# Optimization experiments

Measured on AMD Instinct MI355X. Metric: run time of the kernel, lower is better.

## Reference

```python
import jax, jax.numpy as jnp
import numpy as np

B = 32
T, F1, F2 = 128, 8, 8          # input_shape
N_PATCHES = 1024               # (128/4)*(8/1)*(8/2)
INPUT_D = 8                    # 4*1*2
D = 64                         # hidden_d
H = 8                          # n_heads
DH = D // H                    # d_head = 8
S = N_PATCHES + 1              # sequence length with class token
OUT_D = 9
EPS = 1e-5


def _pos_emb(seq_len, d):
    # Faithful to the original (including the odd-index formula precedence):
    # even j: sin(i / 10000**(j/d));  odd j: cos(i / (10000**(j-1) / d))
    i = np.arange(seq_len, dtype=np.float64)[:, None]
    j = np.arange(d, dtype=np.float64)[None, :]
    even = np.sin(i / np.power(10000.0, j / d))
    odd = np.cos(i / (np.power(10000.0, j - 1.0) / d))
    return jnp.asarray(np.where(j.astype(np.int64) % 2 == 0, even, odd), dtype=jnp.float32)


def _layernorm2d(x, gamma, beta):
    # nn.LayerNorm((S, D)): normalize over the last TWO dims, affine [S, D]
    mu = jnp.mean(x, axis=(-2, -1), keepdims=True)
    var = jnp.mean((x - mu) ** 2, axis=(-2, -1), keepdims=True)
    return (x - mu) * jax.lax.rsqrt(var + EPS) * gamma + beta


def setup_inputs() -> dict:
    key = jax.random.key(0)
    ks = jax.random.split(key, 18)
    sc = 0.05
    return {
        "images": jax.random.normal(ks[0], (B, T, F1, F2), jnp.float32),
        "w_map": jax.random.normal(ks[1], (INPUT_D, D), jnp.float32) * sc,
        "b_map": jax.random.normal(ks[2], (D,), jnp.float32) * sc,
        "cls_tok": jax.random.uniform(ks[3], (1, D), jnp.float32),
        "g1": jnp.ones((S, D), jnp.float32),
        "be1": jnp.zeros((S, D), jnp.float32),
        "wq": jax.random.normal(ks[4], (H, DH, DH), jnp.float32) * sc,
        "bq": jax.random.normal(ks[5], (H, DH), jnp.float32) * sc,
        "wk": jax.random.normal(ks[6], (H, DH, DH), jnp.float32) * sc,
        "bk": jax.random.normal(ks[7], (H, DH), jnp.float32) * sc,
        "wv": jax.random.normal(ks[8], (H, DH, DH), jnp.float32) * sc,
        "bv": jax.random.normal(ks[9], (H, DH), jnp.float32) * sc,
        "g2": jnp.ones((S, D), jnp.float32),
        "be2": jnp.zeros((S, D), jnp.float32),
        "w_enc": jax.random.normal(ks[10], (D, D), jnp.float32) * sc,
        "b_enc": jax.random.normal(ks[11], (D,), jnp.float32) * sc,
        "w_out": jax.random.normal(ks[12], (D, OUT_D), jnp.float32) * sc,
        "b_out": jax.random.normal(ks[13], (OUT_D,), jnp.float32) * sc,
    }


def _msa(x, wq, bq, wk, bk, wv, bv):
    # x: [B, S, D] -> per-head linear QKV, softmax attention, concat heads
    b, s, _ = x.shape
    xh = x.reshape(b, s, H, DH)                                   # [B,S,H,dh]
    q = jnp.einsum("bshd,hde->bshe", xh, wq) + bq
    k = jnp.einsum("bshd,hde->bshe", xh, wk) + bk
    v = jnp.einsum("bshd,hde->bshe", xh, wv) + bv
    scores = jnp.einsum("bqhe,bkhe->bhqk", q, k) / (DH ** 0.5)    # [B,H,S,S]
    attn = jax.nn.softmax(scores, axis=-1)
    out = jnp.einsum("bhqk,bkhe->bqhe", attn, v)                  # [B,S,H,dh]
    return out.reshape(b, s, D)


def reference(images, w_map, b_map, cls_tok, g1, be1, wq, bq, wk, bk, wv, bv,
              g2, be2, w_enc, b_enc, w_out, b_out):
    n = images.shape[0]
    patches = images.reshape(n, N_PATCHES, INPUT_D)
    tokens = patches @ w_map + b_map                              # [B,P,D]
    cls = jnp.broadcast_to(cls_tok[None, :, :], (n, 1, D))
    tokens = jnp.concatenate([cls, tokens], axis=1)               # [B,S,D]
    tokens = tokens + _pos_emb(S, D)[None, :, :]
    out = tokens + _msa(_layernorm2d(tokens, g1, be1), wq, bq, wk, bk, wv, bv)
    out = out + jax.nn.relu(_layernorm2d(out, g2, be2) @ w_enc + b_enc)
    h = out[:, 0]                                                 # class token
    return jax.nn.softmax(h @ w_out + b_out, axis=-1)
```

## Files before the change

### kernel.cpp

```cpp
#include <hip/hip_runtime.h>
#include <math.h>

#define BB 32
#define SS 1025
#define DD 64
#define HH 8
#define IN_D 8
#define NPATCH 1024
#define OUTD 9
#define EPSF 1e-5f
#define SD (SS*DD)
#define SP 1056
#define NQT 65
#define NCH 33
#define VTROW 1064
#define NTB 257
#define ZROW 1055

typedef __attribute__((ext_vector_type(8))) short bf16x8;
typedef __attribute__((ext_vector_type(4))) float f32x4;
typedef __attribute__((ext_vector_type(4))) unsigned u32x4;

#define SCALE_LOG2E (0.35355339059327378f * 1.4426950408889634f)

#if __has_builtin(__builtin_amdgcn_exp2f)
__device__ __forceinline__ float exp2_fast(float x) { return __builtin_amdgcn_exp2f(x); }
#else
__device__ __forceinline__ float exp2_fast(float x) {
    float r; asm("v_exp_f32 %0, %1" : "=v"(r) : "v"(x)); return r;
}
#endif

__device__ __forceinline__ short f2bf(float f) {
    union { float f; unsigned u; } a; a.f = f;
    unsigned r = a.u + 0x7FFFu + ((a.u >> 16) & 1u);
    return (short)(r >> 16);
}

__device__ __forceinline__ unsigned cvt_pk_bf16(float lo, float hi) {
    unsigned r;
    asm("v_cvt_pk_bf16_f32 %0, %1, %2" : "=v"(r) : "v"(lo), "v"(hi));
    return r;
}

__device__ __forceinline__ int sigmaPV(int v) {
    return ((v & 24) >> 1) | (v & 3) | ((v & 4) << 2);
}

__global__ void k_tokens(const float* __restrict__ images, const float* __restrict__ w_map,
                         const float* __restrict__ b_map, const float* __restrict__ cls,
                         float* __restrict__ tokens, float* __restrict__ part1,
                         float* __restrict__ partq1, float* __restrict__ sum2,
                         float* __restrict__ sumsq2) {
    int b = blockIdx.y;
    int bx = blockIdx.x;
    int idx = bx * 256 + threadIdx.x;
    int tid = threadIdx.x;
    __shared__ float recip[64];
    __shared__ float sh[512];
    if (tid < 64) {
        int j = tid;
        float div;
        if ((j & 1) == 0)
            div = powf(10000.0f, (float)j * (1.0f / 64.0f));
        else
            div = powf(10000.0f, (float)(j - 1)) * (1.0f / 64.0f);
        recip[j] = 1.0f / div;
    }
    __syncthreads();
    float lv = 0.f, lvv = 0.f;
    if (idx < SD) {
        int s = idx >> 6, j = idx & 63;
        float arg = (float)s * recip[j];
        float pv = (j & 1) ? __cosf(arg) : __sinf(arg);
        float v;
        if (s == 0) {
            v = cls[j];
        } else {
            const float* p = images + (size_t)b * (NPATCH * IN_D) + (size_t)(s - 1) * IN_D;
            float acc = b_map[j];
#pragma unroll
            for (int i = 0; i < IN_D; ++i) acc += p[i] * w_map[i * DD + j];
            v = acc;
        }
        v += pv;
        tokens[(size_t)b * SD + idx] = v;
        lv = v; lvv = v * v;
    }
    sh[tid] = lv; sh[256 + tid] = lvv;
    __syncthreads();
    for (int off = 128; off > 0; off >>= 1) {
        if (tid < off) { sh[tid] += sh[tid + off]; sh[256 + tid] += sh[256 + tid + off]; }
        __syncthreads();
    }
    if (tid == 0) {
        part1[b * NTB + bx] = sh[0];
        partq1[b * NTB + bx] = sh[256];
    }
    if (bx == 0) {
        if (tid == 0) sum2[b] = 0.f;
        if (tid == 1) sumsq2[b] = 0.f;
    }
}

__global__ void k_qkv(const float* __restrict__ tokens, const float* __restrict__ part1,
                      const float* __restrict__ partq1, const float* __restrict__ g1,
                      const float* __restrict__ be1,
                      const float* __restrict__ wq, const float* __restrict__ bq,
                      const float* __restrict__ wk, const float* __restrict__ bk,
                      const float* __restrict__ wv, const float* __restrict__ bv,
                      short* __restrict__ qb, short* __restrict__ kb, short* __restrict__ vb) {
    int b = blockIdx.y, bx = blockIdx.x, tid = threadIdx.x;
    __shared__ float sh[512];
    __shared__ float xs[4][DD];
    __shared__ float stats[2];
    {
        float s = 0.f, ss = 0.f;
        for (int i = tid; i < NTB; i += 256) { s += part1[b * NTB + i]; ss += partq1[b * NTB + i]; }
        sh[tid] = s; sh[256 + tid] = ss;
        __syncthreads();
        for (int off = 128; off > 0; off >>= 1) {
            if (tid < off) { sh[tid] += sh[tid + off]; sh[256 + tid] += sh[256 + tid + off]; }
            __syncthreads();
        }
        if (tid == 0) {
            float mu = sh[0] / (float)SD;
            float var = sh[256] / (float)SD - mu * mu;
            stats[0] = mu;
            stats[1] = rsqrtf(var + EPSF);
        }
        __syncthreads();
    }
    int r = tid >> 6, d = tid & 63;
    int srow = bx * 4 + r;
    if (srow < SS) {
        float t = tokens[((size_t)b * SS + srow) * DD + d];
        xs[r][d] = (t - stats[0]) * stats[1] * g1[srow * DD + d] + be1[srow * DD + d];
    }
    __syncthreads();
    for (int o = tid; o < 768; o += 256) {
        int rr = o / 192;
        int rem = o % 192;
        int which = rem / 64;
        int he = rem % 64;
        int h = he >> 3, e = he & 7;
        int s2 = bx * 4 + rr;
        if (s2 >= SS) continue;
        const float* w = (which == 0) ? wq : (which == 1) ? wk : wv;
        const float* bias = (which == 0) ? bq : (which == 1) ? bk : bv;
        float acc = bias[he];
#pragma unroll
        for (int dd = 0; dd < 8; ++dd)
            acc += xs[rr][h * 8 + dd] * w[(h * 8 + dd) * 8 + e];
        if (which == 0) acc *= SCALE_LOG2E;
        short* dst = (which == 0) ? qb : (which == 1) ? kb : vb;
        dst[((size_t)(b * HH + h) * SP + s2) * 8 + e] = f2bf(acc);
    }
    if (bx == NTB - 1) {
        for (int i = tid; i < (SP - SS) * HH * 8; i += 256) {
            int rr = i / (HH * 8);
            int he = i % (HH * 8);
            int hh = he >> 3, e = he & 7;
            kb[((size_t)(b * HH + hh) * SP + SS + rr) * 8 + e] = 0;
        }
    }
}

__global__ __launch_bounds__(512, 4)
void k_attn(const short* __restrict__ qb, const short* __restrict__ kb, const short* __restrict__ vb,
            const float* __restrict__ tokens, float* __restrict__ out0,
            float* __restrict__ sum2, float* __restrict__ sumsq2) {
    __shared__ __align__(16) short VTs[9 * VTROW];
    __shared__ __align__(16) float Es[8 * 256];
    int h = blockIdx.y, b = blockIdx.z;
    int bh = b * HH + h;
    int tid = threadIdx.x;
    int wave = tid >> 6, lane = tid & 63;
    int col = lane & 15, quad = lane >> 4;

    bf16x8 z8 = {0, 0, 0, 0, 0, 0, 0, 0};
    {
        const bf16x8* vg = (const bf16x8*)(vb + (size_t)bh * SP * 8);
        for (int i = tid; i < SP; i += 512) {
            int t = (i & ~31) | sigmaPV(i & 31);
            if (t < SS) {
                bf16x8 row = vg[t];
#pragma unroll
                for (int e = 0; e < 8; ++e) VTs[e * VTROW + i] = row[e];
                VTs[8 * VTROW + i] = (short)0x3F80;
            } else {
#pragma unroll
                for (int e = 0; e < 9; ++e) VTs[e * VTROW + i] = 0;
            }
        }
    }
    __syncthreads();

    const short* kg = kb + (size_t)bh * SP * 8;
    const short* kp0 = kg + ((quad == 0) ? col * 8 : ZROW * 8);
    const int kstep = (quad == 0) ? 256 : 0;
    const int koff16 = (quad == 0) ? 128 : 0;
    const short* vbase_l = VTs + (col < 9 ? col : 8) * VTROW + quad * 8;
    float* Ef = Es + wave * 256;

    float lsum = 0.f, lssq = 0.f;
    int slot = blockIdx.x * 8 + wave;

    for (int qt = slot; qt < NQT; qt += 24) {
        bf16x8 qfrag = z8;
        if (quad == 0) qfrag = *(const bf16x8*)(qb + ((size_t)bh * SP + qt * 16 + col) * 8);
        f32x4 o = {0.f, 0.f, 0.f, 0.f};
        const f32x4 zz = {0.f, 0.f, 0.f, 0.f};
        bf16x8 ka = *(const bf16x8*)kp0;
        bf16x8 kb_ = *(const bf16x8*)(kp0 + koff16);
        const short* kptr = kp0 + kstep;
        const short* vptr = vbase_l;
#pragma clang loop unroll(disable)
        for (int ch = 0; ch < NCH; ++ch) {
            bf16x8 vf = *(const bf16x8*)vptr;
            vptr += 32;
            f32x4 s0 = __builtin_amdgcn_mfma_f32_16x16x32_bf16(ka, qfrag, zz, 0, 0, 0);
            f32x4 s1 = __builtin_amdgcn_mfma_f32_16x16x32_bf16(kb_, qfrag, zz, 0, 0, 0);
            ka = *(const bf16x8*)kptr;
            kb_ = *(const bf16x8*)(kptr + koff16);
            kptr += kstep;
            unsigned p0 = cvt_pk_bf16(exp2_fast(s0[0]), exp2_fast(s0[1]));
            unsigned p1 = cvt_pk_bf16(exp2_fast(s0[2]), exp2_fast(s0[3]));
            unsigned p2 = cvt_pk_bf16(exp2_fast(s1[0]), exp2_fast(s1[1]));
            unsigned p3 = cvt_pk_bf16(exp2_fast(s1[2]), exp2_fast(s1[3]));
            u32x4 pu = {p0, p1, p2, p3};
            o = __builtin_amdgcn_mfma_f32_16x16x32_bf16(__builtin_bit_cast(bf16x8, pu), vf, o, 0, 0, 0);
        }
#pragma unroll
        for (int r = 0; r < 4; ++r) Ef[(quad * 4 + r) * 16 + col] = o[r];
#pragma unroll
        for (int pass = 0; pass < 2; ++pass) {
            int idx = lane + pass * 64;
            int qq = idx >> 3, e = idx & 7;
            int qg = qt * 16 + qq;
            if (qg < SS) {
                float num = Ef[qq * 16 + e];
                float l = Ef[qq * 16 + 8];
                float ov = tokens[((size_t)b * SS + qg) * DD + h * 8 + e] + num / l;
                lsum += ov; lssq += ov * ov;
                if (qg == 0) out0[b * DD + h * 8 + e] = ov;
            }
        }
    }

    __syncthreads();
    Es[tid] = lsum; Es[512 + tid] = lssq;
    __syncthreads();
    for (int off = 256; off > 0; off >>= 1) {
        if (tid < off) { Es[tid] += Es[tid + off]; Es[512 + tid] += Es[512 + tid + off]; }
        __syncthreads();
    }
    if (tid == 0) {
        atomicAdd(&sum2[b], Es[0]);
        atomicAdd(&sumsq2[b], Es[512]);
    }
}

__global__ void k_final(const float* __restrict__ out0, const float* __restrict__ sum2,
                        const float* __restrict__ sumsq2, const float* __restrict__ g2,
                        const float* __restrict__ be2, const float* __restrict__ w_enc,
                        const float* __restrict__ b_enc, const float* __restrict__ w_out,
                        const float* __restrict__ b_out, float* __restrict__ out) {
    int b = blockIdx.x;
    int tid = threadIdx.x;
    __shared__ float xn[DD], hsh[DD], logit[OUTD];
    float n = (float)SD;
    float mu = sum2[b] / n;
    float var = sumsq2[b] / n - mu * mu;
    float rs = rsqrtf(var + EPSF);
    float o = out0[b * DD + tid];
    xn[tid] = (o - mu) * rs * g2[tid] + be2[tid];
    __syncthreads();
    float acc = b_enc[tid];
#pragma unroll
    for (int d = 0; d < DD; ++d) acc += xn[d] * w_enc[d * DD + tid];
    hsh[tid] = o + fmaxf(acc, 0.f);
    __syncthreads();
    if (tid < OUTD) {
        float a = b_out[tid];
#pragma unroll
        for (int d = 0; d < DD; ++d) a += hsh[d] * w_out[d * OUTD + tid];
        logit[tid] = a;
    }
    __syncthreads();
    if (tid == 0) {
        float m = logit[0];
        for (int i = 1; i < OUTD; ++i) m = fmaxf(m, logit[i]);
        float p[OUTD]; float ssum = 0.f;
        for (int i = 0; i < OUTD; ++i) { p[i] = expf(logit[i] - m); ssum += p[i]; }
        for (int i = 0; i < OUTD; ++i) out[b * OUTD + i] = p[i] / ssum;
    }
}

extern "C" void kernel_launch(void* const* d_in, const int* in_sizes, int n_in,
                              void* d_out, int out_size, void* d_ws, size_t ws_size,
                              hipStream_t stream) {
    const float* images = (const float*)d_in[0];
    const float* w_map  = (const float*)d_in[1];
    const float* b_map  = (const float*)d_in[2];
    const float* cls    = (const float*)d_in[3];
    const float* g1     = (const float*)d_in[4];
    const float* be1    = (const float*)d_in[5];
    const float* wq     = (const float*)d_in[6];
    const float* bq     = (const float*)d_in[7];
    const float* wk     = (const float*)d_in[8];
    const float* bk     = (const float*)d_in[9];
    const float* wv     = (const float*)d_in[10];
    const float* bv     = (const float*)d_in[11];
    const float* g2     = (const float*)d_in[12];
    const float* be2    = (const float*)d_in[13];
    const float* w_enc  = (const float*)d_in[14];
    const float* b_enc  = (const float*)d_in[15];
    const float* w_out  = (const float*)d_in[16];
    const float* b_out  = (const float*)d_in[17];
    float* out = (float*)d_out;

    float* ws = (float*)d_ws;
    size_t off = 0;
    float* tokens = ws + off; off += (size_t)BB * SD;
    float* out0   = ws + off; off += BB * DD;
    float* part1  = ws + off; off += BB * NTB;
    float* partq1 = ws + off; off += BB * NTB;
    float* sum2   = ws + off; off += BB;
    float* sumsq2 = ws + off; off += BB;
    short* qb = (short*)(ws + off); off += (size_t)BB * HH * SP * 8 / 2;
    short* kb = (short*)(ws + off); off += (size_t)BB * HH * SP * 8 / 2;
    short* vb = (short*)(ws + off); off += (size_t)BB * HH * SP * 8 / 2;

    k_tokens<<<dim3(NTB, BB), 256, 0, stream>>>(images, w_map, b_map, cls, tokens,
                                                part1, partq1, sum2, sumsq2);
    k_qkv<<<dim3(NTB, BB), 256, 0, stream>>>(tokens, part1, partq1, g1, be1,
                                             wq, bq, wk, bk, wv, bv, qb, kb, vb);
    k_attn<<<dim3(3, HH, BB), 512, 0, stream>>>(qb, kb, vb, tokens, out0, sum2, sumsq2);
    k_final<<<BB, DD, 0, stream>>>(out0, sum2, sumsq2, g2, be2, w_enc, b_enc, w_out, b_out, out);
}
```

Baseline: 175.0 us.

## Process two query tiles per wave in attention, add separate LN stats kernel

The attention loop now handles two query tiles per wave at once, sharing each loaded K fragment and V fragment across both tiles' MFMAs. This halves K and V loads per tile and gives the scheduler more independent MFMA work. The first LayerNorm statistics reduction moves out of every k_qkv block into a small k_stats kernel, so it is no longer repeated about 257 times per batch. Block reductions in k_tokens now use wave shuffles instead of a shared-memory tree. The costs are higher register pressure from two accumulators and score sets, a load imbalance for the odd leftover tile, and one extra kernel launch.

Measured after the change: 167.4 us. -4.4%, faster.

```diff
diff --git a/kernel.cpp b/kernel.cpp
--- a/kernel.cpp
+++ b/kernel.cpp
@@ -57,7 +57,7 @@
     int idx = bx * 256 + threadIdx.x;
     int tid = threadIdx.x;
     __shared__ float recip[64];
-    __shared__ float sh[512];
+    __shared__ float wsred[8];
     if (tid < 64) {
         int j = tid;
         float div;
@@ -87,55 +87,59 @@
         tokens[(size_t)b * SD + idx] = v;
         lv = v; lvv = v * v;
     }
-    sh[tid] = lv; sh[256 + tid] = lvv;
-    __syncthreads();
-    for (int off = 128; off > 0; off >>= 1) {
-        if (tid < off) { sh[tid] += sh[tid + off]; sh[256 + tid] += sh[256 + tid + off]; }
-        __syncthreads();
-    }
-    if (tid == 0) {
-        part1[b * NTB + bx] = sh[0];
-        partq1[b * NTB + bx] = sh[256];
-    }
+    for (int off = 32; off > 0; off >>= 1) {
+        lv += __shfl_down(lv, off, 64);
+        lvv += __shfl_down(lvv, off, 64);
+    }
+    int wv = tid >> 6, ln = tid & 63;
+    if (ln == 0) { wsred[wv] = lv; wsred[4 + wv] = lvv; }
+    __syncthreads();
+    if (tid == 0)  part1[b * NTB + bx]  = wsred[0] + wsred[1] + wsred[2] + wsred[3];
+    if (tid == 64) partq1[b * NTB + bx] = wsred[4] + wsred[5] + wsred[6] + wsred[7];
     if (bx == 0) {
         if (tid == 0) sum2[b] = 0.f;
         if (tid == 1) sumsq2[b] = 0.f;
     }
 }
 
-__global__ void k_qkv(const float* __restrict__ tokens, const float* __restrict__ part1,
-                      const float* __restrict__ partq1, const float* __restrict__ g1,
-                      const float* __restrict__ be1,
+__global__ void k_stats(const float* __restrict__ part1, const float* __restrict__ partq1,
+                        float* __restrict__ stats) {
+    int b = blockIdx.x, tid = threadIdx.x;
+    float s = 0.f, ss = 0.f;
+    for (int i = tid; i < NTB; i += 256) { s += part1[b * NTB + i]; ss += partq1[b * NTB + i]; }
+    for (int off = 32; off > 0; off >>= 1) {
+        s += __shfl_down(s, off, 64);
+        ss += __shfl_down(ss, off, 64);
+    }
+    __shared__ float wsred[8];
+    int wv = tid >> 6, ln = tid & 63;
+    if (ln == 0) { wsred[wv] = s; wsred[4 + wv] = ss; }
+    __syncthreads();
+    if (tid == 0) {
+        float t  = wsred[0] + wsred[1] + wsred[2] + wsred[3];
+        float tq = wsred[4] + wsred[5] + wsred[6] + wsred[7];
+        float mu = t / (float)SD;
+        float var = tq / (float)SD - mu * mu;
+        stats[b * 2] = mu;
+        stats[b * 2 + 1] = rsqrtf(var + EPSF);
+    }
+}
+
+__global__ void k_qkv(const float* __restrict__ tokens, const float* __restrict__ stats,
+                      const float* __restrict__ g1, const float* __restrict__ be1,
                       const float* __restrict__ wq, const float* __restrict__ bq,
                       const float* __restrict__ wk, const float* __restrict__ bk,
                       const float* __restrict__ wv, const float* __restrict__ bv,
                       short* __restrict__ qb, short* __restrict__ kb, short* __restrict__ vb) {
     int b = blockIdx.y, bx = blockIdx.x, tid = threadIdx.x;
-    __shared__ float sh[512];
     __shared__ float xs[4][DD];
-    __shared__ float stats[2];
-    {
-        float s = 0.f, ss = 0.f;
-        for (int i = tid; i < NTB; i += 256) { s += part1[b * NTB + i]; ss += partq1[b * NTB + i]; }
-        sh[tid] = s; sh[256 + tid] = ss;
-        __syncthreads();
-        for (int off = 128; off > 0; off >>= 1) {
-            if (tid < off) { sh[tid] += sh[tid + off]; sh[256 + tid] += sh[256 + tid + off]; }
-            __syncthreads();
-        }
-        if (tid == 0) {
-            float mu = sh[0] / (float)SD;
-            float var = sh[256] / (float)SD - mu * mu;
-            stats[0] = mu;
-            stats[1] = rsqrtf(var + EPSF);
-        }
-        __syncthreads();
-    }
+    float mu = stats[b * 2];
+    float rsig = stats[b * 2 + 1];
     int r = tid >> 6, d = tid & 63;
     int srow = bx * 4 + r;
     if (srow < SS) {
         float t = tokens[((size_t)b * SS + srow) * DD + d];
-        xs[r][d] = (t - stats[0]) * stats[1] * g1[srow * DD + d] + be1[srow * DD + d];
+        xs[r][d] = (t - mu) * rsig * g1[srow * DD + d] + be1[srow * DD + d];
     }
     __syncthreads();
     for (int o = tid; o < 768; o += 256) {
@@ -166,6 +170,33 @@
     }
 }
 
+#define PACK_PV(s0, s1, o, vf) do { \
+    unsigned p0_ = cvt_pk_bf16(exp2_fast((s0)[0]), exp2_fast((s0)[1])); \
+    unsigned p1_ = cvt_pk_bf16(exp2_fast((s0)[2]), exp2_fast((s0)[3])); \
+    unsigned p2_ = cvt_pk_bf16(exp2_fast((s1)[0]), exp2_fast((s1)[1])); \
+    unsigned p3_ = cvt_pk_bf16(exp2_fast((s1)[2]), exp2_fast((s1)[3])); \
+    u32x4 pu_ = {p0_, p1_, p2_, p3_}; \
+    (o) = __builtin_amdgcn_mfma_f32_16x16x32_bf16(__builtin_bit_cast(bf16x8, pu_), (vf), (o), 0, 0, 0); \
+} while (0)
+
+#define EPILOGUE(qt, o) do { \
+    _Pragma("unroll") \
+    for (int r_ = 0; r_ < 4; ++r_) Ef[(quad * 4 + r_) * 16 + col] = (o)[r_]; \
+    _Pragma("unroll") \
+    for (int pass_ = 0; pass_ < 2; ++pass_) { \
+        int idx_ = lane + pass_ * 64; \
+        int qq_ = idx_ >> 3, e_ = idx_ & 7; \
+        int qg_ = (qt) * 16 + qq_; \
+        if (qg_ < SS) { \
+            float num_ = Ef[qq_ * 16 + e_]; \
+            float l_ = Ef[qq_ * 16 + 8]; \
+            float ov_ = tokens[((size_t)b * SS + qg_) * DD + h * 8 + e_] + num_ / l_; \
+            lsum += ov_; lssq += ov_ * ov_; \
+            if (qg_ == 0) out0[b * DD + h * 8 + e_] = ov_; \
+        } \
+    } \
+} while (0)
+
 __global__ __launch_bounds__(512, 4)
 void k_attn(const short* __restrict__ qb, const short* __restrict__ kb, const short* __restrict__ vb,
             const float* __restrict__ tokens, float* __restrict__ out0,
@@ -206,45 +237,55 @@
     float lsum = 0.f, lssq = 0.f;
     int slot = blockIdx.x * 8 + wave;
 
-    for (int qt = slot; qt < NQT; qt += 24) {
-        bf16x8 qfrag = z8;
-        if (quad == 0) qfrag = *(const bf16x8*)(qb + ((size_t)bh * SP + qt * 16 + col) * 8);
-        f32x4 o = {0.f, 0.f, 0.f, 0.f};
-        const f32x4 zz = {0.f, 0.f, 0.f, 0.f};
-        bf16x8 ka = *(const bf16x8*)kp0;
-        bf16x8 kb_ = *(const bf16x8*)(kp0 + koff16);
-        const short* kptr = kp0 + kstep;
-        const short* vptr = vbase_l;
+    const f32x4 zz = {0.f, 0.f, 0.f, 0.f};
+    for (int qt0 = slot; qt0 < NQT; qt0 += 48) {
+        int qt1 = qt0 + 24;
+        bf16x8 qf0 = z8;
+        if (quad == 0) qf0 = *(const bf16x8*)(qb + ((size_t)bh * SP + qt0 * 16 + col) * 8);
+        if (qt1 < NQT) {
+            bf16x8 qf1 = z8;
+            if (quad == 0) qf1 = *(const bf16x8*)(qb + ((size_t)bh * SP + qt1 * 16 + col) * 8);
+            f32x4 oa = zz, ob = zz;
+            const short* kptr = kp0;
+            bf16x8 ka = *(const bf16x8*)kptr;
+            bf16x8 kbx = *(const bf16x8*)(kptr + koff16);
+            kptr += kstep;
+            const short* vptr = vbase_l;
 #pragma clang loop unroll(disable)
-        for (int ch = 0; ch < NCH; ++ch) {
-            bf16x8 vf = *(const bf16x8*)vptr;
-            vptr += 32;
-            f32x4 s0 = __builtin_amdgcn_mfma_f32_16x16x32_bf16(ka, qfrag, zz, 0, 0, 0);
-            f32x4 s1 = __builtin_amdgcn_mfma_f32_16x16x32_bf16(kb_, qfrag, zz, 0, 0, 0);
-            ka = *(const bf16x8*)kptr;
-            kb_ = *(const bf16x8*)(kptr + koff16);
+            for (int ch = 0; ch < NCH; ++ch) {
+                bf16x8 vf = *(const bf16x8*)vptr;
+                vptr += 32;
+                f32x4 s0a = __builtin_amdgcn_mfma_f32_16x16x32_bf16(ka, qf0, zz, 0, 0, 0);
+                f32x4 s1a = __builtin_amdgcn_mfma_f32_16x16x32_bf16(kbx, qf0, zz, 0, 0, 0);
+                f32x4 s0b = __builtin_amdgcn_mfma_f32_16x16x32_bf16(ka, qf1, zz, 0, 0, 0);
+                f32x4 s1b = __builtin_amdgcn_mfma_f32_16x16x32_bf16(kbx, qf1, zz, 0, 0, 0);
+                ka = *(const bf16x8*)kptr;
+                kbx = *(const bf16x8*)(kptr + koff16);
+                kptr += kstep;
+                PACK_PV(s0a, s1a, oa, vf);
+                PACK_PV(s0b, s1b, ob, vf);
+            }
+            EPILOGUE(qt0, oa);
+            EPILOGUE(qt1, ob);
+        } else {
+            f32x4 oa = zz;
+            const short* kptr = kp0;
+            bf16x8 ka = *(const bf16x8*)kptr;
+            bf16x8 kbx = *(const bf16x8*)(kptr + koff16);
             kptr += kstep;
-            unsigned p0 = cvt_pk_bf16(exp2_fast(s0[0]), exp2_fast(s0[1]));
-            unsigned p1 = cvt_pk_bf16(exp2_fast(s0[2]), exp2_fast(s0[3]));
-            unsigned p2 = cvt_pk_bf16(exp2_fast(s1[0]), exp2_fast(s1[1]));
-            unsigned p3 = cvt_pk_bf16(exp2_fast(s1[2]), exp2_fast(s1[3]));
-            u32x4 pu = {p0, p1, p2, p3};
-            o = __builtin_amdgcn_mfma_f32_16x16x32_bf16(__builtin_bit_cast(bf16x8, pu), vf, o, 0, 0, 0);
-        }
-#pragma unroll
-        for (int r = 0; r < 4; ++r) Ef[(quad * 4 + r) * 16 + col] = o[r];
-#pragma unroll
-        for (int pass = 0; pass < 2; ++pass) {
-            int idx = lane + pass * 64;
-            int qq = idx >> 3, e = idx & 7;
-            int qg = qt * 16 + qq;
-            if (qg < SS) {
-                float num = Ef[qq * 16 + e];
-                float l = Ef[qq * 16 + 8];
-                float ov = tokens[((size_t)b * SS + qg) * DD + h * 8 + e] + num / l;
-                lsum += ov; lssq += ov * ov;
-                if (qg == 0) out0[b * DD + h * 8 + e] = ov;
+            const short* vptr = vbase_l;
+#pragma clang loop unroll(disable)
+            for (int ch = 0; ch < NCH; ++ch) {
+                bf16x8 vf = *(const bf16x8*)vptr;
+                vptr += 32;
+                f32x4 s0a = __builtin_amdgcn_mfma_f32_16x16x32_bf16(ka, qf0, zz, 0, 0, 0);
+                f32x4 s1a = __builtin_amdgcn_mfma_f32_16x16x32_bf16(kbx, qf0, zz, 0, 0, 0);
+                ka = *(const bf16x8*)kptr;
+                kbx = *(const bf16x8*)(kptr + koff16);
+                kptr += kstep;
+                PACK_PV(s0a, s1a, oa, vf);
             }
+            EPILOGUE(qt0, oa);
         }
     }
 
@@ -328,13 +369,15 @@
     float* partq1 = ws + off; off += BB * NTB;
     float* sum2   = ws + off; off += BB;
     float* sumsq2 = ws + off; off += BB;
+    float* stats  = ws + off; off += 2 * BB;
     short* qb = (short*)(ws + off); off += (size_t)BB * HH * SP * 8 / 2;
     short* kb = (short*)(ws + off); off += (size_t)BB * HH * SP * 8 / 2;
     short* vb = (short*)(ws + off); off += (size_t)BB * HH * SP * 8 / 2;
 
     k_tokens<<<dim3(NTB, BB), 256, 0, stream>>>(images, w_map, b_map, cls, tokens,
                                                 part1, partq1, sum2, sumsq2);
-    k_qkv<<<dim3(NTB, BB), 256, 0, stream>>>(tokens, part1, partq1, g1, be1,
+    k_stats<<<BB, 256, 0, stream>>>(part1, partq1, stats);
+    k_qkv<<<dim3(NTB, BB), 256, 0, stream>>>(tokens, stats, g1, be1,
                                              wq, bq, wk, bk, wv, bv, qb, kb, vb);
     k_attn<<<dim3(3, HH, BB), 512, 0, stream>>>(qb, kb, vb, tokens, out0, sum2, sumsq2);
     k_final<<<BB, DD, 0, stream>>>(out0, sum2, sumsq2, g2, be2, w_enc, b_enc, w_out, b_out, out);
```
